# Kernel tuning notes

Measured on AMD Instinct MI355X. Metric: run time of the kernel, lower is better.

The kernel has to match this reference:

```python
import jax, jax.numpy as jnp
import numpy as np

D = 256; NH = 8; NL = 4; NP = 4; DFF = 1024; BS = 8; NQ = 300
DH = D // NH
EPS = 1e-5
SPATIAL = np.array([[100, 150], [50, 75], [25, 38], [13, 19]], dtype=np.int64)  # (H, W) per level
SIZES = (SPATIAL[:, 0] * SPATIAL[:, 1])
S = int(SIZES.sum())  # 19947
LSI = np.concatenate([[0], np.cumsum(SIZES)[:-1]]).astype(np.int64)


def setup_inputs() -> dict:
    key = jax.random.key(0)
    ks = iter(jax.random.split(key, 48))
    def nrm(shape, s=0.02):
        return jax.random.normal(next(ks), shape, jnp.float32) * s
    return {
        "tgt": jax.random.normal(next(ks), (BS, NQ, D), jnp.float32),
        "tgt_query_pos": jax.random.normal(next(ks), (BS, NQ, D), jnp.float32),
        "tgt_reference_points": jax.random.uniform(next(ks), (BS, NQ, NL, 2), jnp.float32),
        "memory": jax.random.normal(next(ks), (BS, S, D), jnp.float32),
        "memory_key_padding_mask": jnp.zeros((BS, S), jnp.bool_),
        "memory_spatial_shapes": jnp.asarray(SPATIAL),
        "memory_level_start_index": jnp.asarray(LSI),
        # self-attention (nn.MultiheadAttention) params
        "in_proj_w": nrm((3 * D, D)), "in_proj_b": jnp.zeros((3 * D,), jnp.float32),
        "out_proj_w": nrm((D, D)), "out_proj_b": jnp.zeros((D,), jnp.float32),
        # layernorms
        "norm1_g": jnp.ones((D,), jnp.float32), "norm1_b": jnp.zeros((D,), jnp.float32),
        "norm2_g": jnp.ones((D,), jnp.float32), "norm2_b": jnp.zeros((D,), jnp.float32),
        "norm3_g": jnp.ones((D,), jnp.float32), "norm3_b": jnp.zeros((D,), jnp.float32),
        # MSDeformAttn params
        "samp_off_w": nrm((NH * NL * NP * 2, D)), "samp_off_b": nrm((NH * NL * NP * 2,), 0.5),
        "attn_wt_w": nrm((NH * NL * NP, D)), "attn_wt_b": jnp.zeros((NH * NL * NP,), jnp.float32),
        "value_w": nrm((D, D)), "value_b": jnp.zeros((D,), jnp.float32),
        "outp_w": nrm((D, D)), "outp_b": jnp.zeros((D,), jnp.float32),
        # FFN params
        "lin1_w": nrm((DFF, D)), "lin1_b": jnp.zeros((DFF,), jnp.float32),
        "lin2_w": nrm((D, DFF)), "lin2_b": jnp.zeros((D,), jnp.float32),
    }


def _ln(x, g, b):
    m = x.mean(-1, keepdims=True)
    v = ((x - m) ** 2).mean(-1, keepdims=True)
    return (x - m) / jnp.sqrt(v + EPS) * g + b


def _self_attn(tgt, pos, in_w, in_b, ow, ob):
    bs, nq, _ = tgt.shape
    qk = tgt + pos
    qw, kw, vw = jnp.split(in_w, 3, axis=0)
    qb, kb, vb = jnp.split(in_b, 3)
    proj = lambda x, w, b: (x @ w.T + b).reshape(bs, nq, NH, DH)
    qh, kh, vh = proj(qk, qw, qb), proj(qk, kw, kb), proj(tgt, vw, vb)
    logits = jnp.einsum('bqhd,bkhd->bhqk', qh, kh) / np.sqrt(DH).astype(np.float32)
    a = jax.nn.softmax(logits, axis=-1)
    o = jnp.einsum('bhqk,bkhd->bqhd', a, vh).reshape(bs, nq, D)
    return o @ ow.T + ob


def _msdeform(query, ref, memory, pad_mask, so_w, so_b, aw_w, aw_b, vw, vb, ow, ob):
    bs, nq, _ = query.shape
    value = memory @ vw.T + vb
    value = jnp.where(pad_mask[..., None], 0.0, value).reshape(bs, S, NH, DH)
    off = (query @ so_w.T + so_b).reshape(bs, nq, NH, NL, NP, 2)
    aw = jax.nn.softmax((query @ aw_w.T + aw_b).reshape(bs, nq, NH, NL * NP), axis=-1)
    aw = aw.reshape(bs, nq, NH, NL, NP)
    # offset normalizer is (W, H) per level
    normalizer = jnp.asarray(SPATIAL[:, ::-1].copy(), jnp.float32)
    locs = ref[:, :, None, :, None, :] + off / normalizer[None, None, None, :, None, :]
    out = jnp.zeros((bs, nq, NH, DH), jnp.float32)
    for l in range(NL):
        Hl, Wl = int(SPATIAL[l, 0]), int(SPATIAL[l, 1])
        s0 = int(LSI[l])
        v = value[:, s0:s0 + Hl * Wl]  # [bs, Hl*Wl, NH, DH]
        # grid_sample(align_corners=False) pixel mapping
        x = locs[:, :, :, l, :, 0] * Wl - 0.5  # [bs, nq, NH, NP]
        y = locs[:, :, :, l, :, 1] * Hl - 0.5
        x0f, y0f = jnp.floor(x), jnp.floor(y)
        tx, ty = x - x0f, y - y0f
        x0, y0 = x0f.astype(jnp.int32), y0f.astype(jnp.int32)
        samp = jnp.zeros(x.shape + (DH,), jnp.float32)
        for dy, dx, w in ((0, 0, (1 - ty) * (1 - tx)), (0, 1, (1 - ty) * tx),
                          (1, 0, ty * (1 - tx)), (1, 1, ty * tx)):
            xi, yi = x0 + dx, y0 + dy
            valid = (xi >= 0) & (xi < Wl) & (yi >= 0) & (yi < Hl)  # zero padding
            idx = jnp.clip(yi, 0, Hl - 1) * Wl + jnp.clip(xi, 0, Wl - 1)
            idx2 = idx.swapaxes(2, 3).reshape(bs, nq * NP, NH)
            g = jnp.take_along_axis(v, idx2[..., None], axis=1)  # [bs, nq*NP, NH, DH]
            g = g.reshape(bs, nq, NP, NH, DH).transpose(0, 1, 3, 2, 4)
            samp = samp + g * (w * valid)[..., None]
        out = out + jnp.einsum('bqhp,bqhpd->bqhd', aw[:, :, :, l], samp)
    return out.reshape(bs, nq, D) @ ow.T + ob


def reference(tgt, tgt_query_pos, tgt_reference_points, memory, memory_key_padding_mask,
              memory_spatial_shapes, memory_level_start_index,
              in_proj_w, in_proj_b, out_proj_w, out_proj_b,
              norm1_g, norm1_b, norm2_g, norm2_b, norm3_g, norm3_b,
              samp_off_w, samp_off_b, attn_wt_w, attn_wt_b,
              value_w, value_b, outp_w, outp_b,
              lin1_w, lin1_b, lin2_w, lin2_b):
    # self-cross ordering (self_cross=True), eval mode (dropout=identity)
    t2 = _self_attn(tgt, tgt_query_pos, in_proj_w, in_proj_b, out_proj_w, out_proj_b)
    tgt = _ln(tgt + t2, norm2_g, norm2_b)
    t2 = _msdeform(tgt + tgt_query_pos, tgt_reference_points, memory, memory_key_padding_mask,
                   samp_off_w, samp_off_b, attn_wt_w, attn_wt_b, value_w, value_b, outp_w, outp_b)
    tgt = _ln(tgt + t2, norm1_g, norm1_b)
    t2 = jax.nn.relu(tgt @ lin1_w.T + lin1_b) @ lin2_w.T + lin2_b
    return _ln(tgt + t2, norm3_g, norm3_b)
```

## Files before the change

### kernel.cpp

```cpp
#include <hip/hip_runtime.h>
#include <hip/hip_bf16.h>

#define D_   256
#define NH_  8
#define NL_  4
#define NP_  4
#define DFF_ 1024
#define BS_  8
#define NQ_  300
#define DH_  32
#define S_TOT 19947
#define EPS_ 1e-5f

typedef __bf16 bf16x8 __attribute__((ext_vector_type(8)));
typedef __bf16 bf16x4 __attribute__((ext_vector_type(4)));
typedef float  f32x4  __attribute__((ext_vector_type(4)));

#define W_INW  0
#define W_OUTW 196608
#define W_SOW  262144
#define W_AWW  327680
#define W_VW   360448
#define W_OPW  425984
#define W_L1W  491520
#define W_L2W  753664
#define W_TOT  1015808

__global__ __launch_bounds__(256) void cast_w_kernel(
    const float* __restrict__ s_inw, const float* __restrict__ s_outw,
    const float* __restrict__ s_sow, const float* __restrict__ s_aww,
    const float* __restrict__ s_vw,  const float* __restrict__ s_opw,
    const float* __restrict__ s_l1w, const float* __restrict__ s_l2w,
    __bf16* __restrict__ dst)
{
    const int i = (blockIdx.x * 256 + threadIdx.x) * 4;
    if (i >= W_TOT) return;
    const float* s; int off;
    if      (i < W_OUTW) { s = s_inw;  off = W_INW;  }
    else if (i < W_SOW)  { s = s_outw; off = W_OUTW; }
    else if (i < W_AWW)  { s = s_sow;  off = W_SOW;  }
    else if (i < W_VW)   { s = s_aww;  off = W_AWW;  }
    else if (i < W_OPW)  { s = s_vw;   off = W_VW;   }
    else if (i < W_L1W)  { s = s_opw;  off = W_OPW;  }
    else if (i < W_L2W)  { s = s_l1w;  off = W_L1W;  }
    else                 { s = s_l2w;  off = W_L2W;  }
    const float4 v = *(const float4*)(s + (i - off));
    bf16x4 o;
    o[0] = (__bf16)v.x; o[1] = (__bf16)v.y;
    o[2] = (__bf16)v.z; o[3] = (__bf16)v.w;
    *(bf16x4*)(dst + i) = o;
}

__global__ __launch_bounds__(256) void rearrange_vw_kernel(
    const __bf16* __restrict__ W, __bf16* __restrict__ Wf)
{
    const int g = blockIdx.x * 256 + threadIdx.x;
    const int l = g & 63;
    const int t = (g >> 6) & 15;
    const int s = g >> 10;
    const int row = t * 16 + (l & 15);
    const int col = s * 32 + (l >> 4) * 8;
    *(bf16x8*)(Wf + (size_t)g * 8) = *(const bf16x8*)(W + (size_t)row * 256 + col);
}

__global__ __launch_bounds__(256, 8) void gemm_value(
    const float* __restrict__ A, const __bf16* __restrict__ Wf,
    const float* __restrict__ bias, __hip_bfloat16* __restrict__ C, int M)
{
    __shared__ __align__(16) __bf16 As[16][264];
    const int tid = threadIdx.x;
    const int wave = tid >> 6, lane = tid & 63;
    const int m0 = blockIdx.x * 16;
    const int frow = lane & 15;
    const int k8 = (lane >> 4) * 8;

    const int c0 = (tid * 4) & 255;
#pragma unroll
    for (int i = 0; i < 4; ++i) {
        const int r = (tid >> 6) + 4 * i;
        int gr = m0 + r; if (gr >= M) gr = M - 1;
        const float4 a = *(const float4*)(A + (size_t)gr * 256 + c0);
        bf16x4 o;
        o[0] = (__bf16)a.x; o[1] = (__bf16)a.y;
        o[2] = (__bf16)a.z; o[3] = (__bf16)a.w;
        *(bf16x4*)&As[r][c0] = o;
    }
    __syncthreads();

    f32x4 acc[4];
#pragma unroll
    for (int j = 0; j < 4; ++j) acc[j] = (f32x4){0.f, 0.f, 0.f, 0.f};

    const __bf16* bbase = Wf + ((size_t)(wave * 4) * 64 + lane) * 8;

#pragma unroll
    for (int s = 0; s < 8; ++s) {
        bf16x8 bF[4];
        const __bf16* bp = bbase + (size_t)s * 8192;
#pragma unroll
        for (int j = 0; j < 4; ++j)
            bF[j] = *(const bf16x8*)(bp + j * 512);

        const bf16x8 aF = *(const bf16x8*)&As[frow][s * 32 + k8];

#pragma unroll
        for (int j = 0; j < 4; ++j)
            acc[j] = __builtin_amdgcn_mfma_f32_16x16x32_bf16(aF, bF[j], acc[j], 0, 0, 0);
    }

    const int row0 = m0 + (lane >> 4) * 4;
#pragma unroll
    for (int j = 0; j < 4; ++j) {
        const int col = wave * 64 + j * 16 + frow;
        const float bb = bias[col];
#pragma unroll
        for (int r = 0; r < 4; ++r)
            if (row0 + r < M)
                C[(size_t)(row0 + r) * 256 + col] = __float2bfloat16(acc[j][r] + bb);
    }
}

__global__ __launch_bounds__(256) void gemm_small(
    const float* __restrict__ A, const float* __restrict__ A2,
    const __bf16* __restrict__ W, const float* __restrict__ bias,
    float* __restrict__ C, int M, int N, int K, int relu)
{
    __shared__ __align__(16) __bf16 As[64][40];
    __shared__ __align__(16) __bf16 Bs[64][40];
    const int tid = threadIdx.x;
    const int wave = tid >> 6, lane = tid & 63;
    const int m0 = blockIdx.x * 64, n0 = blockIdx.y * 64;
    const int frow = lane & 15, fk = (lane >> 4) * 8;

    f32x4 acc[4];
#pragma unroll
    for (int j = 0; j < 4; ++j) acc[j] = (f32x4){0.f, 0.f, 0.f, 0.f};

    const int ar = tid >> 2;
    const int ak = (tid & 3) * 8;
    const bool a_ok = (m0 + ar) < M;

    for (int k0 = 0; k0 < K; k0 += 32) {
        float4 a0 = make_float4(0,0,0,0), a1 = a0;
        if (a_ok) {
            const float* ap = A + (size_t)(m0 + ar) * K + k0 + ak;
            a0 = *(const float4*)ap;
            a1 = *(const float4*)(ap + 4);
            if (A2) {
                const float* ap2 = A2 + (size_t)(m0 + ar) * K + k0 + ak;
                const float4 c0 = *(const float4*)ap2;
                const float4 c1 = *(const float4*)(ap2 + 4);
                a0.x += c0.x; a0.y += c0.y; a0.z += c0.z; a0.w += c0.w;
                a1.x += c1.x; a1.y += c1.y; a1.z += c1.z; a1.w += c1.w;
            }
        }
        const bf16x8 b8 = *(const bf16x8*)(W + (size_t)(n0 + ar) * K + k0 + ak);

        __syncthreads();
        bf16x8 w0;
        w0[0] = (__bf16)a0.x; w0[1] = (__bf16)a0.y; w0[2] = (__bf16)a0.z; w0[3] = (__bf16)a0.w;
        w0[4] = (__bf16)a1.x; w0[5] = (__bf16)a1.y; w0[6] = (__bf16)a1.z; w0[7] = (__bf16)a1.w;
        *(bf16x8*)&As[ar][ak] = w0;
        *(bf16x8*)&Bs[ar][ak] = b8;
        __syncthreads();

        const bf16x8 aF = *(const bf16x8*)&As[wave * 16 + frow][fk];
#pragma unroll
        for (int j = 0; j < 4; ++j) {
            const bf16x8 bF = *(const bf16x8*)&Bs[j * 16 + frow][fk];
            acc[j] = __builtin_amdgcn_mfma_f32_16x16x32_bf16(aF, bF, acc[j], 0, 0, 0);
        }
    }

    const int row = m0 + wave * 16 + (lane >> 4) * 4;
#pragma unroll
    for (int j = 0; j < 4; ++j) {
        const int col = n0 + j * 16 + frow;
        const float bb = bias[col];
#pragma unroll
        for (int r = 0; r < 4; ++r) {
            if (row + r >= M) continue;
            float val = acc[j][r] + bb;
            if (relu) val = fmaxf(val, 0.f);
            C[(size_t)(row + r) * N + col] = val;
        }
    }
}

__global__ __launch_bounds__(256) void attn_logits_kernel(
    const float* __restrict__ qk, __bf16* __restrict__ P)
{
    const int qt = blockIdx.x, bh = blockIdx.y;
    const int b = bh >> 3, h = bh & 7;
    const int wave = threadIdx.x >> 6, lane = threadIdx.x & 63;
    const int m = qt * 64 + wave * 16 + (lane & 15);
    const int k8 = (lane >> 4) * 8;
    const float scale = 0.17677669529663687f;

    bf16x8 aF = {};
    if (m < NQ_) {
        const float* qp = qk + (size_t)(b * NQ_ + m) * 512 + h * 32 + k8;
        const float4 q0 = *(const float4*)qp;
        const float4 q1 = *(const float4*)(qp + 4);
        aF[0] = (__bf16)q0.x; aF[1] = (__bf16)q0.y;
        aF[2] = (__bf16)q0.z; aF[3] = (__bf16)q0.w;
        aF[4] = (__bf16)q1.x; aF[5] = (__bf16)q1.y;
        aF[6] = (__bf16)q1.z; aF[7] = (__bf16)q1.w;
    }

    f32x4 c[19];
#pragma unroll
    for (int t = 0; t < 19; ++t) {
        const int n = t * 16 + (lane & 15);
        bf16x8 bF = {};
        if (n < NQ_) {
            const float* kp = qk + (size_t)(b * NQ_ + n) * 512 + 256 + h * 32 + k8;
            const float4 k0 = *(const float4*)kp;
            const float4 k1 = *(const float4*)(kp + 4);
            bF[0] = (__bf16)k0.x; bF[1] = (__bf16)k0.y;
            bF[2] = (__bf16)k0.z; bF[3] = (__bf16)k0.w;
            bF[4] = (__bf16)k1.x; bF[5] = (__bf16)k1.y;
            bF[6] = (__bf16)k1.z; bF[7] = (__bf16)k1.w;
        }
        f32x4 z = (f32x4){0.f, 0.f, 0.f, 0.f};
        c[t] = __builtin_amdgcn_mfma_f32_16x16x32_bf16(aF, bF, z, 0, 0, 0);
    }

    const int myc = lane & 15;
#pragma unroll
    for (int t = 0; t < 19; ++t) {
        const bool ok = (t * 16 + myc) < NQ_;
#pragma unroll
        for (int r = 0; r < 4; ++r)
            c[t][r] = ok ? c[t][r] * scale : -1e30f;
    }

    float mx[4] = {-1e30f, -1e30f, -1e30f, -1e30f};
#pragma unroll
    for (int t = 0; t < 19; ++t)
#pragma unroll
        for (int r = 0; r < 4; ++r) mx[r] = fmaxf(mx[r], c[t][r]);
#pragma unroll
    for (int off = 8; off; off >>= 1)
#pragma unroll
        for (int r = 0; r < 4; ++r)
            mx[r] = fmaxf(mx[r], __shfl_xor(mx[r], off, 64));

    float sum[4] = {0.f, 0.f, 0.f, 0.f};
#pragma unroll
    for (int t = 0; t < 19; ++t)
#pragma unroll
        for (int r = 0; r < 4; ++r) {
            const float e = __expf(c[t][r] - mx[r]);
            c[t][r] = e;
            sum[r] += e;
        }
#pragma unroll
    for (int off = 8; off; off >>= 1)
#pragma unroll
        for (int r = 0; r < 4; ++r)
            sum[r] += __shfl_xor(sum[r], off, 64);
    float inv[4];
#pragma unroll
    for (int r = 0; r < 4; ++r) inv[r] = 1.f / sum[r];

    __bf16* Pr = P + (size_t)bh * NQ_ * 320;
    const int row0 = qt * 64 + wave * 16 + (lane >> 4) * 4;
#pragma unroll
    for (int t = 0; t < 19; ++t) {
        const int col = t * 16 + myc;
        if (col >= NQ_) continue;
#pragma unroll
        for (int r = 0; r < 4; ++r)
            if (row0 + r < NQ_)
                Pr[(size_t)(row0 + r) * 320 + col] = (__bf16)(c[t][r] * inv[r]);
    }
}

__global__ __launch_bounds__(256) void attn_pv_kernel(
    const __bf16* __restrict__ P, const float* __restrict__ v,
    float* __restrict__ attn)
{
    __shared__ __align__(16) __bf16 Vt[32][328];
    const int qt = blockIdx.x, bh = blockIdx.y;
    const int b = bh >> 3, h = bh & 7;
    const int tid = threadIdx.x;

    {
        const int d = tid & 31;
        for (int kk = tid >> 5; kk < NQ_; kk += 8)
            Vt[d][kk] = (__bf16)v[(size_t)(b * NQ_ + kk) * 256 + h * 32 + d];
        for (int i = tid; i < 32 * 20; i += 256)
            Vt[i & 31][300 + (i >> 5)] = (__bf16)0.f;
    }
    __syncthreads();

    const int wave = tid >> 6, lane = tid & 63;
    const int mrow = qt * 64 + wave * 16 + (lane & 15);
    const int k8 = (lane >> 4) * 8;
    const __bf16* Pr = P + (size_t)bh * NQ_ * 320;

    f32x4 acc0 = (f32x4){0.f, 0.f, 0.f, 0.f};
    f32x4 acc1 = acc0;
#pragma unroll
    for (int k0 = 0; k0 < 320; k0 += 32) {
        bf16x8 aF = {};
        if (mrow < NQ_) aF = *(const bf16x8*)(Pr + (size_t)mrow * 320 + k0 + k8);
        const bf16x8 b0 = *(const bf16x8*)&Vt[lane & 15][k0 + k8];
        const bf16x8 b1 = *(const bf16x8*)&Vt[16 + (lane & 15)][k0 + k8];
        acc0 = __builtin_amdgcn_mfma_f32_16x16x32_bf16(aF, b0, acc0, 0, 0, 0);
        acc1 = __builtin_amdgcn_mfma_f32_16x16x32_bf16(aF, b1, acc1, 0, 0, 0);
    }

    const int row0 = qt * 64 + wave * 16 + (lane >> 4) * 4;
    const int col = lane & 15;
#pragma unroll
    for (int r = 0; r < 4; ++r) {
        if (row0 + r >= NQ_) continue;
        float* op = attn + (size_t)(b * NQ_ + row0 + r) * 256 + h * 32;
        op[col]      = acc0[r];
        op[col + 16] = acc1[r];
    }
}

__global__ __launch_bounds__(256) void ln_kernel(
    const float* __restrict__ x, const float* __restrict__ res,
    const float* __restrict__ g, const float* __restrict__ bt,
    float* __restrict__ out,
    const float* __restrict__ pos, float* __restrict__ out2)
{
    const int row = blockIdx.x;
    const int tid = threadIdx.x;
    const size_t idx = (size_t)row * D_ + tid;
    float v = x[idx] + (res ? res[idx] : 0.f);

    __shared__ float red[4];
    float s = v;
#pragma unroll
    for (int off = 32; off; off >>= 1) s += __shfl_xor(s, off, 64);
    if ((tid & 63) == 0) red[tid >> 6] = s;
    __syncthreads();
    const float mean = (red[0] + red[1] + red[2] + red[3]) * (1.f / D_);
    const float c = v - mean;
    __syncthreads();

    float s2 = c * c;
#pragma unroll
    for (int off = 32; off; off >>= 1) s2 += __shfl_xor(s2, off, 64);
    if ((tid & 63) == 0) red[tid >> 6] = s2;
    __syncthreads();
    const float var = (red[0] + red[1] + red[2] + red[3]) * (1.f / D_);

    const float y = c * rsqrtf(var + EPS_) * g[tid] + bt[tid];
    out[idx] = y;
    if (out2) out2[idx] = y + pos[idx];
}

__global__ __launch_bounds__(256) void msdeform_kernel(
    const float* __restrict__ offs, const float* __restrict__ awl,
    const float* __restrict__ refp, const __hip_bfloat16* __restrict__ value,
    float* __restrict__ samp)
{
    const int row = blockIdx.x;
    const int b = row / NQ_;
    const int tid = threadIdx.x;
    const int h = tid >> 5, d = tid & 31;

    __shared__ float off_s[256];
    __shared__ float aw_s[128];
    __shared__ float ref_s[8];
    off_s[tid] = offs[(size_t)row * 256 + tid];
    if (tid < 128) aw_s[tid] = awl[(size_t)row * 128 + tid];
    if (tid < 8) ref_s[tid] = refp[(size_t)row * 8 + tid];
    __syncthreads();

    float mx = -1e30f;
#pragma unroll
    for (int i = 0; i < 16; ++i) mx = fmaxf(mx, aw_s[h * 16 + i]);
    float sum = 0.f;
#pragma unroll
    for (int i = 0; i < 16; ++i) sum += __expf(aw_s[h * 16 + i] - mx);
    const float winv = 1.f / sum;

    const int Hs[4] = {100, 50, 25, 13};
    const int Wl_[4] = {150, 75, 38, 19};
    const int S0[4] = {0, 15000, 18750, 19700};

    float o = 0.f;
    const __hip_bfloat16* vbase = value + ((size_t)b * S_TOT) * D_ + h * 32 + d;

#pragma unroll
    for (int l = 0; l < NL_; ++l) {
        const int Hl = Hs[l], Wl = Wl_[l];
        const float rx = ref_s[l * 2], ry = ref_s[l * 2 + 1];
        const __hip_bfloat16* vl = vbase + (size_t)S0[l] * D_;
#pragma unroll
        for (int p = 0; p < NP_; ++p) {
            const int oi = ((h * NL_ + l) * NP_ + p) * 2;
            const float lx = rx + off_s[oi] / (float)Wl;
            const float ly = ry + off_s[oi + 1] / (float)Hl;
            const float x = lx * Wl - 0.5f;
            const float y = ly * Hl - 0.5f;
            const float x0f = floorf(x), y0f = floorf(y);
            const float tx = x - x0f, ty = y - y0f;
            const int x0 = (int)x0f, y0 = (int)y0f;
            const float aw = __expf(aw_s[h * 16 + l * 4 + p] - mx) * winv;

            float sacc = 0.f;
#pragma unroll
            for (int cc = 0; cc < 4; ++cc) {
                const int dy = cc >> 1, dx = cc & 1;
                const int xi = x0 + dx, yi = y0 + dy;
                const float w = (dy ? ty : 1.f - ty) * (dx ? tx : 1.f - tx);
                if (xi >= 0 && xi < Wl && yi >= 0 && yi < Hl) {
                    const int idx = yi * Wl + xi;
                    sacc += w * __bfloat162float(vl[(size_t)idx * D_]);
                }
            }
            o += aw * sacc;
        }
    }
    samp[(size_t)row * 256 + tid] = o;
}

extern "C" void kernel_launch(void* const* d_in, const int* in_sizes, int n_in,
                              void* d_out, int out_size, void* d_ws, size_t ws_size,
                              hipStream_t stream)
{
    const float* tgt   = (const float*)d_in[0];
    const float* pos   = (const float*)d_in[1];
    const float* refp  = (const float*)d_in[2];
    const float* memory= (const float*)d_in[3];
    const float* in_w  = (const float*)d_in[7];
    const float* in_b  = (const float*)d_in[8];
    const float* outw  = (const float*)d_in[9];
    const float* outb  = (const float*)d_in[10];
    const float* n1g = (const float*)d_in[11]; const float* n1b = (const float*)d_in[12];
    const float* n2g = (const float*)d_in[13]; const float* n2b = (const float*)d_in[14];
    const float* n3g = (const float*)d_in[15]; const float* n3b = (const float*)d_in[16];
    const float* sow = (const float*)d_in[17]; const float* sob = (const float*)d_in[18];
    const float* aww = (const float*)d_in[19]; const float* awb = (const float*)d_in[20];
    const float* vw  = (const float*)d_in[21]; const float* vb_ = (const float*)d_in[22];
    const float* opw = (const float*)d_in[23]; const float* opb = (const float*)d_in[24];
    const float* l1w = (const float*)d_in[25]; const float* l1b = (const float*)d_in[26];
    const float* l2w = (const float*)d_in[27]; const float* l2b = (const float*)d_in[28];
    float* out = (float*)d_out;

    char* ws = (char*)d_ws;
    size_t o = 0;
    auto alloc = [&](size_t bytes) -> char* {
        char* p = ws + o;
        o += (bytes + 255) & ~(size_t)255;
        return p;
    };

    const int M = BS_ * NQ_;
    __bf16* Wb = (__bf16*)alloc((size_t)W_TOT * 2);
    __bf16* Wf = (__bf16*)alloc((size_t)65536 * 2);
    __hip_bfloat16* value = (__hip_bfloat16*)alloc((size_t)BS_ * S_TOT * D_ * 2);
    __bf16* P    = (__bf16*)alloc((size_t)64 * NQ_ * 320 * 2);
    float* qk    = (float*)alloc((size_t)M * 512 * 4);
    float* v     = (float*)alloc((size_t)M * 256 * 4);
    float* attn  = (float*)alloc((size_t)M * 256 * 4);
    float* attno = (float*)alloc((size_t)M * 256 * 4);
    float* tgt1  = (float*)alloc((size_t)M * 256 * 4);
    float* query2= (float*)alloc((size_t)M * 256 * 4);
    float* offs  = (float*)alloc((size_t)M * 256 * 4);
    float* awl   = (float*)alloc((size_t)M * 128 * 4);
    float* samp  = (float*)alloc((size_t)M * 256 * 4);
    float* t2m   = (float*)alloc((size_t)M * 256 * 4);
    float* tgt2  = (float*)alloc((size_t)M * 256 * 4);
    float* ffn1  = (float*)alloc((size_t)M * 1024 * 4);
    float* ffn2  = (float*)alloc((size_t)M * 256 * 4);

    const dim3 blk(256);
    const int MB = (M + 63) / 64;
    const int MV16 = (BS_ * S_TOT + 15) / 16;

    cast_w_kernel<<<(W_TOT / 4 + 255) / 256, blk, 0, stream>>>(
        in_w, outw, sow, aww, vw, opw, l1w, l2w, Wb);
    rearrange_vw_kernel<<<32, blk, 0, stream>>>(Wb + W_VW, Wf);

    gemm_small<<<dim3(MB, 8), blk, 0, stream>>>(tgt, pos, Wb + W_INW, in_b, qk, M, 512, 256, 0);
    gemm_small<<<dim3(MB, 4), blk, 0, stream>>>(tgt, nullptr, Wb + W_INW + 512 * 256, in_b + 512, v, M, 256, 256, 0);
    attn_logits_kernel<<<dim3(5, 64), blk, 0, stream>>>(qk, P);
    attn_pv_kernel<<<dim3(5, 64), blk, 0, stream>>>(P, v, attn);
    gemm_small<<<dim3(MB, 4), blk, 0, stream>>>(attn, nullptr, Wb + W_OUTW, outb, attno, M, 256, 256, 0);
    ln_kernel<<<M, blk, 0, stream>>>(tgt, attno, n2g, n2b, tgt1, pos, query2);

    gemm_small<<<dim3(MB, 4), blk, 0, stream>>>(query2, nullptr, Wb + W_SOW, sob, offs, M, 256, 256, 0);
    gemm_small<<<dim3(MB, 2), blk, 0, stream>>>(query2, nullptr, Wb + W_AWW, awb, awl, M, 128, 256, 0);
    gemm_value<<<dim3(MV16), blk, 0, stream>>>(memory, Wf, vb_, value, BS_ * S_TOT);
    msdeform_kernel<<<M, blk, 0, stream>>>(offs, awl, refp, value, samp);
    gemm_small<<<dim3(MB, 4), blk, 0, stream>>>(samp, nullptr, Wb + W_OPW, opb, t2m, M, 256, 256, 0);
    ln_kernel<<<M, blk, 0, stream>>>(tgt1, t2m, n1g, n1b, tgt2, nullptr, nullptr);

    gemm_small<<<dim3(MB, 16), blk, 0, stream>>>(tgt2, nullptr, Wb + W_L1W, l1b, ffn1, M, 1024, 256, 1);
    gemm_small<<<dim3(MB, 4), blk, 0, stream>>>(ffn1, nullptr, Wb + W_L2W, l2b, ffn2, M, 256, 1024, 0);
    ln_kernel<<<M, blk, 0, stream>>>(tgt2, ffn2, n3g, n3b, out, nullptr, nullptr);
}
```

Before: 514.2 us.

## Make value projection GEMM persistent with register-resident weights and double-buffered A

Result: faster. 476.8 us (-7.3%).

```diff
diff --git a/kernel.cpp b/kernel.cpp
--- a/kernel.cpp
+++ b/kernel.cpp
@@ -63,60 +63,91 @@
     *(bf16x8*)(Wf + (size_t)g * 8) = *(const bf16x8*)(W + (size_t)row * 256 + col);
 }
 
-__global__ __launch_bounds__(256, 8) void gemm_value(
+__global__ __launch_bounds__(512, 4) void gemm_value(
     const float* __restrict__ A, const __bf16* __restrict__ Wf,
     const float* __restrict__ bias, __hip_bfloat16* __restrict__ C, int M)
 {
-    __shared__ __align__(16) __bf16 As[16][264];
+    __shared__ __align__(16) __bf16 As[2][16][264];
     const int tid = threadIdx.x;
     const int wave = tid >> 6, lane = tid & 63;
-    const int m0 = blockIdx.x * 16;
     const int frow = lane & 15;
     const int k8 = (lane >> 4) * 8;
 
-    const int c0 = (tid * 4) & 255;
-#pragma unroll
-    for (int i = 0; i < 4; ++i) {
-        const int r = (tid >> 6) + 4 * i;
-        int gr = m0 + r; if (gr >= M) gr = M - 1;
-        const float4 a = *(const float4*)(A + (size_t)gr * 256 + c0);
-        bf16x4 o;
-        o[0] = (__bf16)a.x; o[1] = (__bf16)a.y;
-        o[2] = (__bf16)a.z; o[3] = (__bf16)a.w;
-        *(bf16x4*)&As[r][c0] = o;
+    bf16x8 bB[2][8];
+#pragma unroll
+    for (int j = 0; j < 2; ++j) {
+        const int t = wave * 2 + j;
+#pragma unroll
+        for (int s = 0; s < 8; ++s)
+            bB[j][s] = *(const bf16x8*)(Wf + ((size_t)(s * 16 + t) * 64 + lane) * 8);
+    }
+    float bb0 = bias[wave * 32 + frow];
+    float bb1 = bias[wave * 32 + 16 + frow];
+
+    const int nt = (M + 15) >> 4;
+    const int stride = gridDim.x;
+    int tile = blockIdx.x;
+
+    const int srow = tid >> 5;
+    const int scol = (tid & 31) * 8;
+
+    {
+        int gr = tile * 16 + srow; if (gr >= M) gr = M - 1;
+        const float* ap = A + (size_t)gr * 256 + scol;
+        const float4 a0 = *(const float4*)ap;
+        const float4 a1 = *(const float4*)(ap + 4);
+        bf16x8 o;
+        o[0] = (__bf16)a0.x; o[1] = (__bf16)a0.y;
+        o[2] = (__bf16)a0.z; o[3] = (__bf16)a0.w;
+        o[4] = (__bf16)a1.x; o[5] = (__bf16)a1.y;
+        o[6] = (__bf16)a1.z; o[7] = (__bf16)a1.w;
+        *(bf16x8*)&As[0][srow][scol] = o;
     }
     __syncthreads();
 
-    f32x4 acc[4];
-#pragma unroll
-    for (int j = 0; j < 4; ++j) acc[j] = (f32x4){0.f, 0.f, 0.f, 0.f};
-
-    const __bf16* bbase = Wf + ((size_t)(wave * 4) * 64 + lane) * 8;
-
-#pragma unroll
-    for (int s = 0; s < 8; ++s) {
-        bf16x8 bF[4];
-        const __bf16* bp = bbase + (size_t)s * 8192;
-#pragma unroll
-        for (int j = 0; j < 4; ++j)
-            bF[j] = *(const bf16x8*)(bp + j * 512);
-
-        const bf16x8 aF = *(const bf16x8*)&As[frow][s * 32 + k8];
-
-#pragma unroll
-        for (int j = 0; j < 4; ++j)
-            acc[j] = __builtin_amdgcn_mfma_f32_16x16x32_bf16(aF, bF[j], acc[j], 0, 0, 0);
-    }
-
-    const int row0 = m0 + (lane >> 4) * 4;
-#pragma unroll
-    for (int j = 0; j < 4; ++j) {
-        const int col = wave * 64 + j * 16 + frow;
-        const float bb = bias[col];
-#pragma unroll
-        for (int r = 0; r < 4; ++r)
-            if (row0 + r < M)
-                C[(size_t)(row0 + r) * 256 + col] = __float2bfloat16(acc[j][r] + bb);
+    int buf = 0;
+    for (; tile < nt; tile += stride, buf ^= 1) {
+        const int nxt = tile + stride;
+        const bool have_nxt = nxt < nt;
+        float4 p0, p1;
+        if (have_nxt) {
+            int gr = nxt * 16 + srow; if (gr >= M) gr = M - 1;
+            const float* ap = A + (size_t)gr * 256 + scol;
+            p0 = *(const float4*)ap;
+            p1 = *(const float4*)(ap + 4);
+        }
+
+        f32x4 acc0 = (f32x4){0.f, 0.f, 0.f, 0.f};
+        f32x4 acc1 = acc0;
+#pragma unroll
+        for (int s = 0; s < 8; ++s) {
+            const bf16x8 aF = *(const bf16x8*)&As[buf][frow][s * 32 + k8];
+            acc0 = __builtin_amdgcn_mfma_f32_16x16x32_bf16(aF, bB[0][s], acc0, 0, 0, 0);
+            acc1 = __builtin_amdgcn_mfma_f32_16x16x32_bf16(aF, bB[1][s], acc1, 0, 0, 0);
+        }
+
+        const int m0 = tile * 16;
+        const int row0 = (lane >> 4) * 4;
+        const int col0 = wave * 32 + frow;
+#pragma unroll
+        for (int r = 0; r < 4; ++r) {
+            const int gr = m0 + row0 + r;
+            if (gr < M) {
+                __hip_bfloat16* cp = C + (size_t)gr * 256 + col0;
+                cp[0]  = __float2bfloat16(acc0[r] + bb0);
+                cp[16] = __float2bfloat16(acc1[r] + bb1);
+            }
+        }
+
+        if (have_nxt) {
+            bf16x8 o;
+            o[0] = (__bf16)p0.x; o[1] = (__bf16)p0.y;
+            o[2] = (__bf16)p0.z; o[3] = (__bf16)p0.w;
+            o[4] = (__bf16)p1.x; o[5] = (__bf16)p1.y;
+            o[6] = (__bf16)p1.z; o[7] = (__bf16)p1.w;
+            *(bf16x8*)&As[buf ^ 1][srow][scol] = o;
+        }
+        __syncthreads();
     }
 }
 
@@ -475,7 +506,6 @@
 
     const dim3 blk(256);
     const int MB = (M + 63) / 64;
-    const int MV16 = (BS_ * S_TOT + 15) / 16;
 
     cast_w_kernel<<<(W_TOT / 4 + 255) / 256, blk, 0, stream>>>(
         in_w, outw, sow, aww, vw, opw, l1w, l2w, Wb);
@@ -490,7 +520,7 @@
 
     gemm_small<<<dim3(MB, 4), blk, 0, stream>>>(query2, nullptr, Wb + W_SOW, sob, offs, M, 256, 256, 0);
     gemm_small<<<dim3(MB, 2), blk, 0, stream>>>(query2, nullptr, Wb + W_AWW, awb, awl, M, 128, 256, 0);
-    gemm_value<<<dim3(MV16), blk, 0, stream>>>(memory, Wf, vb_, value, BS_ * S_TOT);
+    gemm_value<<<dim3(512), dim3(512), 0, stream>>>(memory, Wf, vb_, value, BS_ * S_TOT);
     msdeform_kernel<<<M, blk, 0, stream>>>(offs, awl, refp, value, samp);
     gemm_small<<<dim3(MB, 4), blk, 0, stream>>>(samp, nullptr, Wb + W_OPW, opb, t2m, M, 256, 256, 0);
     ln_kernel<<<M, blk, 0, stream>>>(tgt1, t2m, n1g, n1b, tgt2, nullptr, nullptr);
```
